# Performance work log

Hardware: AMD Instinct MI355X
Metric: run time of the kernel (lower is better)

Reference implementation:

```python
import jax, jax.numpy as jnp
import numpy as np
import math

S, B, H, NH = 2048, 1, 4096, 32
HD = H // NH          # 128 head dim
ROT = HD // 2         # 64 rotary dim per half (position_encoding_2d)


def _rotary_tables(seq_len):
    inv_freq = 1.0 / (10000.0 ** (jnp.arange(0, ROT, 2, dtype=jnp.float32) / ROT))  # [ROT/2]
    t = jnp.arange(seq_len, dtype=jnp.float32)
    freqs = jnp.einsum('i,j->ij', t, inv_freq)          # [S, ROT/2]
    emb = jnp.concatenate([freqs, freqs], axis=-1)       # [S, ROT]
    return jnp.cos(emb), jnp.sin(emb)


def _rotate_half(x):
    half = x.shape[-1] // 2
    return jnp.concatenate([-x[..., half:], x[..., :half]], axis=-1)


def _apply_rotary(q, k, cos, sin, pos):
    # q,k: [s,b,nh,ROT]; pos: [s,b]
    c = cos[pos][:, :, None, :]   # [s,b,1,ROT]
    s_ = sin[pos][:, :, None, :]
    return q * c + _rotate_half(q) * s_, k * c + _rotate_half(k) * s_


def reference(hidden_states, position_ids, attention_mask, layer_id, w_qkv, b_qkv, w_dense, b_dense):
    s, b, _ = hidden_states.shape
    # fused QKV projection (Linear: x @ W.T + b)
    qkv = jnp.einsum('sbh,oh->sbo', hidden_states, w_qkv) + b_qkv     # [s,b,3H]
    qkv = qkv.reshape(s, b, NH, 3 * HD)
    q, k, v = jnp.split(qkv, 3, axis=-1)                               # each [s,b,nh,HD]
    # 2D rotary: split head dim in two halves, rotate with pos / block pos ids
    cos, sin = _rotary_tables(s)
    pos = position_ids[:, 0, :].T        # [s,b]
    blk = position_ids[:, 1, :].T        # [s,b]
    q1, q2 = jnp.split(q, 2, axis=-1)
    k1, k2 = jnp.split(k, 2, axis=-1)
    q1, k1 = _apply_rotary(q1, k1, cos, sin, pos)
    q2, k2 = _apply_rotary(q2, k2, cos, sin, blk)
    q = jnp.concatenate([q1, q2], axis=-1)
    k = jnp.concatenate([k1, k2], axis=-1)
    # layer-id-dependent scaling (GLM numerics): q scaled down by coeff, logits scaled back up
    coeff = float(layer_id + 1)
    q = q / (math.sqrt(HD) * coeff)
    scores = jnp.einsum('sbnd,tbnd->bnst', q, k)                       # [b,nh,s,s]
    scores = jnp.where(attention_mask, jnp.asarray(-10000.0, scores.dtype), scores)
    probs = jax.nn.softmax(scores.astype(jnp.float32) * coeff, axis=-1).astype(scores.dtype)
    ctx = jnp.einsum('bnst,tbnd->sbnd', probs, v).reshape(s, b, H)     # [s,b,H]
    return jnp.einsum('sbh,oh->sbo', ctx, w_dense) + b_dense


def setup_inputs() -> dict:
    key = jax.random.key(0)
    k1, k2, k3, k4, k5, k6 = jax.random.split(key, 6)
    init = 0.02
    hidden_states = jax.random.normal(k1, (S, B, H), dtype=jnp.float32)
    # GLM-style 2D position ids: [B, 2, S] (row 0: positions, row 1: block positions)
    pos = jnp.broadcast_to(jnp.arange(S, dtype=jnp.int64), (B, S))
    blk = jnp.broadcast_to(jnp.arange(S, dtype=jnp.int64), (B, S))
    position_ids = jnp.stack([pos, blk], axis=1)                        # [B,2,S]
    # causal mask: True = masked (future positions)
    causal = jnp.triu(jnp.ones((S, S), dtype=bool), k=1)
    attention_mask = jnp.broadcast_to(causal[None, None], (B, 1, S, S))
    return {
        'hidden_states': hidden_states,
        'position_ids': position_ids,
        'attention_mask': attention_mask,
        'layer_id': 5,
        'w_qkv': jax.random.normal(k2, (3 * H, H), dtype=jnp.float32) * init,
        'b_qkv': jax.random.normal(k3, (3 * H,), dtype=jnp.float32) * init,
        'w_dense': jax.random.normal(k4, (H, H), dtype=jnp.float32) * init,
        'b_dense': jax.random.normal(k5, (H,), dtype=jnp.float32) * init,
    }
```

## Files before the change

kernel.cpp:

```cpp
#include <hip/hip_runtime.h>
#include <math.h>
#include <stdint.h>

constexpr int S  = 2048;
constexpr int H  = 4096;
constexpr int NH = 32;
constexpr int HD = 128;
constexpr int H3 = 3 * H;

typedef unsigned short u16;
typedef __bf16 bf16x8 __attribute__((ext_vector_type(8)));
typedef float  f32x4  __attribute__((ext_vector_type(4)));
typedef unsigned short us8 __attribute__((ext_vector_type(8)));

__device__ __forceinline__ u16 f2bf(float f) {
  uint32_t u = __float_as_uint(f);
  uint32_t r = (u + 0x7fff + ((u >> 16) & 1)) >> 16;
  return (u16)r;
}
__device__ __forceinline__ float bf2f(u16 u) {
  return __uint_as_float((uint32_t)u << 16);
}

__device__ __forceinline__ void load_lds16(const void* g, void* l) {
  __builtin_amdgcn_global_load_lds(
      (__attribute__((address_space(1))) void*)(uintptr_t)g,
      (__attribute__((address_space(3))) void*)l,
      16, 0, 0);
}

#define SBAR0 __builtin_amdgcn_sched_barrier(0)

__global__ __launch_bounds__(256)
void cast_all(const float* __restrict__ w_qkv, const float* __restrict__ hidden,
              const float* __restrict__ w_dense, u16* __restrict__ wq,
              u16* __restrict__ hb, u16* __restrict__ wd) {
  constexpr int NQ  = H3 * H / 4;
  constexpr int NHd = S * H / 4;
  constexpr int ND  = H * H / 4;
  constexpr int NT  = NQ + NHd + ND;
  for (int i = blockIdx.x * 256 + threadIdx.x; i < NT; i += gridDim.x * 256) {
    const float4* src;
    ushort4* dst;
    int j = i;
    if (j < NQ)            { src = (const float4*)w_qkv;  dst = (ushort4*)wq; }
    else if (j < NQ + NHd) { j -= NQ; src = (const float4*)hidden; dst = (ushort4*)hb; }
    else                   { j -= NQ + NHd; src = (const float4*)w_dense; dst = (ushort4*)wd; }
    float4 v = src[j];
    ushort4 o;
    o.x = f2bf(v.x); o.y = f2bf(v.y); o.z = f2bf(v.z); o.w = f2bf(v.w);
    dst[j] = o;
  }
}

template<int STRIDE, int OUT_BF16>
__global__ __launch_bounds__(512, 2)
void gemm256(const u16* __restrict__ A, const u16* __restrict__ W,
             const float* __restrict__ bias, void* __restrict__ Cout) {
  constexpr int K   = 4096;
  constexpr int NT  = K / 64;
  constexpr int NTM = 8;
  constexpr int TB  = 65536;
  __shared__ __attribute__((aligned(16))) unsigned char lds[2 * TB];
  const int tid = threadIdx.x, wave = tid >> 6, lane = tid & 63;
  const int l15 = lane & 15, l4 = lane >> 4;
  const int wr = wave >> 2, wc = wave & 3;

  const int nwg = gridDim.x, bid = blockIdx.x;
  const int cpx = nwg >> 3;
  const int swz = (bid & 7) * cpx + (bid >> 3);
  const int bx = swz / NTM, by = swz - bx * NTM;
  const int bm = by * 256, bn = bx * 256;

  const int srow = lane >> 3;
  const int sck  = ((lane & 7) ^ srow) * 8;
  const u16* Abase = A + (size_t)(bm + srow) * K + sck;
  const u16* Wbase = W + (size_t)(bn + srow) * K + sck;

  auto stageU = [&](int tt, int u) {
    const int b = tt & 1;
    if (u < 4) {
      const int rb = u * 64 + wave * 8;
      load_lds16(Abase + (size_t)rb * K + tt * 64, &lds[b * TB + rb * 128]);
    } else {
      const int rb = (u - 4) * 64 + wave * 8;
      load_lds16(Wbase + (size_t)rb * K + tt * 64,
                 &lds[b * TB + 32768 + rb * 128]);
    }
  };

  f32x4 acc[8][4];
#pragma unroll
  for (int i = 0; i < 8; ++i)
#pragma unroll
    for (int j = 0; j < 4; ++j) acc[i][j] = (f32x4)0.f;

#pragma unroll
  for (int u = 0; u < 8; ++u) stageU(0, u);
#pragma unroll
  for (int u = 0; u < 8; ++u) stageU(1, u);
  asm volatile("s_waitcnt vmcnt(8)" ::: "memory");
  SBAR0;
  __builtin_amdgcn_s_barrier();

  const int arow = wr * 128 + l15;
  const int brow = wc * 64 + l15;
  const int ckx  = l15 & 7;

  bf16x8 af[4][2], bfA[2][2], bfB[2][2];

  for (int t = 0; t < NT; ++t) {
    const int b0 = (t & 1) * TB;
    const bool st = (t + 2 < NT);
#pragma unroll
    for (int mi = 0; mi < 4; ++mi)
#pragma unroll
      for (int ks = 0; ks < 2; ++ks)
        af[mi][ks] = *(const bf16x8*)&lds[b0 + (arow + mi * 16) * 128 +
                                          (((ks * 4 + l4) ^ ckx) * 16)];
#pragma unroll
    for (int ni = 0; ni < 2; ++ni)
#pragma unroll
      for (int ks = 0; ks < 2; ++ks)
        bfA[ni][ks] = *(const bf16x8*)&lds[b0 + 32768 + (brow + ni * 16) * 128 +
                                           (((ks * 4 + l4) ^ ckx) * 16)];
    SBAR0; __builtin_amdgcn_s_barrier();
    asm volatile("s_waitcnt lgkmcnt(0)" ::: "memory");
    SBAR0;
    __builtin_amdgcn_s_setprio(1);
#pragma unroll
    for (int ks = 0; ks < 2; ++ks)
#pragma unroll
      for (int mi = 0; mi < 4; ++mi)
#pragma unroll
        for (int ni = 0; ni < 2; ++ni)
          acc[mi][ni] = __builtin_amdgcn_mfma_f32_16x16x32_bf16(af[mi][ks], bfA[ni][ks], acc[mi][ni], 0, 0, 0);
    __builtin_amdgcn_s_setprio(0);
    SBAR0; __builtin_amdgcn_s_barrier();
#pragma unroll
    for (int ni = 0; ni < 2; ++ni)
#pragma unroll
      for (int ks = 0; ks < 2; ++ks)
        bfB[ni][ks] = *(const bf16x8*)&lds[b0 + 32768 + (brow + (ni + 2) * 16) * 128 +
                                           (((ks * 4 + l4) ^ ckx) * 16)];
    if (st) { stageU(t + 2, 0); stageU(t + 2, 2); }
    SBAR0; __builtin_amdgcn_s_barrier();
    asm volatile("s_waitcnt lgkmcnt(0)" ::: "memory");
    SBAR0;
    __builtin_amdgcn_s_setprio(1);
#pragma unroll
    for (int ks = 0; ks < 2; ++ks)
#pragma unroll
      for (int mi = 0; mi < 4; ++mi)
#pragma unroll
        for (int ni = 0; ni < 2; ++ni)
          acc[mi][ni + 2] = __builtin_amdgcn_mfma_f32_16x16x32_bf16(af[mi][ks], bfB[ni][ks], acc[mi][ni + 2], 0, 0, 0);
    __builtin_amdgcn_s_setprio(0);
    SBAR0; __builtin_amdgcn_s_barrier();
#pragma unroll
    for (int mi = 0; mi < 4; ++mi)
#pragma unroll
      for (int ks = 0; ks < 2; ++ks)
        af[mi][ks] = *(const bf16x8*)&lds[b0 + (arow + (mi + 4) * 16) * 128 +
                                          (((ks * 4 + l4) ^ ckx) * 16)];
    if (st) { stageU(t + 2, 4); stageU(t + 2, 5); }
    SBAR0; __builtin_amdgcn_s_barrier();
    asm volatile("s_waitcnt lgkmcnt(0)" ::: "memory");
    SBAR0;
    __builtin_amdgcn_s_setprio(1);
#pragma unroll
    for (int ks = 0; ks < 2; ++ks)
#pragma unroll
      for (int mi = 0; mi < 4; ++mi)
#pragma unroll
        for (int ni = 0; ni < 2; ++ni)
          acc[mi + 4][ni] = __builtin_amdgcn_mfma_f32_16x16x32_bf16(af[mi][ks], bfA[ni][ks], acc[mi + 4][ni], 0, 0, 0);
    __builtin_amdgcn_s_setprio(0);
    SBAR0; __builtin_amdgcn_s_barrier();
    if (st) { stageU(t + 2, 1); stageU(t + 2, 3); stageU(t + 2, 6); stageU(t + 2, 7); }
    SBAR0;
    __builtin_amdgcn_s_setprio(1);
#pragma unroll
    for (int ks = 0; ks < 2; ++ks)
#pragma unroll
      for (int mi = 0; mi < 4; ++mi)
#pragma unroll
        for (int ni = 0; ni < 2; ++ni)
          acc[mi + 4][ni + 2] = __builtin_amdgcn_mfma_f32_16x16x32_bf16(af[mi][ks], bfB[ni][ks], acc[mi + 4][ni + 2], 0, 0, 0);
    __builtin_amdgcn_s_setprio(0);
    if (t < NT - 2)       asm volatile("s_waitcnt vmcnt(8)" ::: "memory");
    else if (t == NT - 2) asm volatile("s_waitcnt vmcnt(0)" ::: "memory");
    SBAR0;
    if (t < NT - 1) __builtin_amdgcn_s_barrier();
  }

#pragma unroll
  for (int ni = 0; ni < 4; ++ni) {
    const int col = bn + wc * 64 + ni * 16 + l15;
    const float bv = bias[col];
#pragma unroll
    for (int mi = 0; mi < 8; ++mi) {
#pragma unroll
      for (int r = 0; r < 4; ++r) {
        const int row = bm + wr * 128 + mi * 16 + l4 * 4 + r;
        const float v = acc[mi][ni][r] + bv;
        if (OUT_BF16) ((u16*)Cout)[(size_t)row * STRIDE + col] = f2bf(v);
        else          ((float*)Cout)[(size_t)row * STRIDE + col] = v;
      }
    }
  }
}

template<int STRIDE, int OUT_BF16>
__global__ __launch_bounds__(512, 2)
void gemm8p(const u16* __restrict__ A, const u16* __restrict__ W,
            const float* __restrict__ bias, void* __restrict__ Cout) {
  constexpr int K  = 4096;
  constexpr int NT = K / 64;
  constexpr int NTM = 16;
  constexpr int TB = 49152;
  __shared__ __attribute__((aligned(16))) unsigned char lds[3 * TB];
  const int tid = threadIdx.x, wave = tid >> 6, lane = tid & 63;
  const int l15 = lane & 15, l4 = lane >> 4;
  const int wr = wave >> 2, wc = wave & 3;

  const int nwg = gridDim.x, bid = blockIdx.x;
  const int cpx = nwg >> 3;
  const int swz = (bid & 7) * cpx + (bid >> 3);
  const int bx = swz / NTM, by = swz - bx * NTM;
  const int bm = by * 128, bn = bx * 256;

  const int srow = lane >> 3;
  const int sck  = ((lane & 7) ^ srow) * 8;
  const u16* Abase = A + (size_t)(bm + srow) * K + sck;
  const u16* Wbase = W + (size_t)(bn + srow) * K + sck;

  auto stageA = [&](int tt, int b) {
#pragma unroll
    for (int j = 0; j < 2; ++j) {
      const int rb = j * 64 + wave * 8;
      load_lds16(Abase + (size_t)rb * K + tt * 64, &lds[b * TB + rb * 128]);
    }
  };
  auto stageB = [&](int tt, int b, int u) {
#pragma unroll
    for (int j = 0; j < 2; ++j) {
      const int rb = u * 128 + j * 64 + wave * 8;
      load_lds16(Wbase + (size_t)rb * K + tt * 64,
                 &lds[b * TB + 16384 + rb * 128]);
    }
  };

  f32x4 acc[4][4];
#pragma unroll
  for (int i = 0; i < 4; ++i)
#pragma unroll
    for (int j = 0; j < 4; ++j) acc[i][j] = (f32x4)0.f;

  stageA(0, 0); stageB(0, 0, 0); stageB(0, 0, 1);
  stageA(1, 1); stageB(1, 1, 0); stageB(1, 1, 1);
  asm volatile("s_waitcnt vmcnt(6)" ::: "memory");
  SBAR0;
  __builtin_amdgcn_s_barrier();

  const int arow = wr * 64 + l15;
  const int brow = wc * 64 + l15;
  const int ckx  = l15 & 7;

  bf16x8 af[4][2], bf[4][2];

  int br = 0, bs = 2;
  for (int t = 0; t < NT; ++t) {
    const int b0 = br * TB;
#pragma unroll
    for (int mi = 0; mi < 2; ++mi)
#pragma unroll
      for (int ks = 0; ks < 2; ++ks)
        af[mi][ks] = *(const bf16x8*)&lds[b0 + (arow + mi * 16) * 128 +
                                          (((ks * 4 + l4) ^ ckx) * 16)];
#pragma unroll
    for (int ni = 0; ni < 2; ++ni)
#pragma unroll
      for (int ks = 0; ks < 2; ++ks)
        bf[ni][ks] = *(const bf16x8*)&lds[b0 + 16384 + (brow + ni * 16) * 128 +
                                          (((ks * 4 + l4) ^ ckx) * 16)];
    if (t < NT - 2) stageA(t + 2, bs);
    SBAR0; __builtin_amdgcn_s_barrier();
    asm volatile("s_waitcnt lgkmcnt(0)" ::: "memory");
    SBAR0;
    __builtin_amdgcn_s_setprio(1);
#pragma unroll
    for (int ks = 0; ks < 2; ++ks)
#pragma unroll
      for (int mi = 0; mi < 2; ++mi)
#pragma unroll
        for (int ni = 0; ni < 2; ++ni)
          acc[mi][ni] = __builtin_amdgcn_mfma_f32_16x16x32_bf16(af[mi][ks], bf[ni][ks], acc[mi][ni], 0, 0, 0);
    __builtin_amdgcn_s_setprio(0);
    SBAR0; __builtin_amdgcn_s_barrier();
#pragma unroll
    for (int ni = 2; ni < 4; ++ni)
#pragma unroll
      for (int ks = 0; ks < 2; ++ks)
        bf[ni][ks] = *(const bf16x8*)&lds[b0 + 16384 + (brow + ni * 16) * 128 +
                                          (((ks * 4 + l4) ^ ckx) * 16)];
    if (t < NT - 2) stageB(t + 2, bs, 0);
    SBAR0; __builtin_amdgcn_s_barrier();
    asm volatile("s_waitcnt lgkmcnt(0)" ::: "memory");
    SBAR0;
    __builtin_amdgcn_s_setprio(1);
#pragma unroll
    for (int ks = 0; ks < 2; ++ks)
#pragma unroll
      for (int mi = 0; mi < 2; ++mi)
#pragma unroll
        for (int ni = 2; ni < 4; ++ni)
          acc[mi][ni] = __builtin_amdgcn_mfma_f32_16x16x32_bf16(af[mi][ks], bf[ni][ks], acc[mi][ni], 0, 0, 0);
    __builtin_amdgcn_s_setprio(0);
    SBAR0; __builtin_amdgcn_s_barrier();
#pragma unroll
    for (int mi = 2; mi < 4; ++mi)
#pragma unroll
      for (int ks = 0; ks < 2; ++ks)
        af[mi][ks] = *(const bf16x8*)&lds[b0 + (arow + mi * 16) * 128 +
                                          (((ks * 4 + l4) ^ ckx) * 16)];
    if (t < NT - 2) stageB(t + 2, bs, 1);
    SBAR0; __builtin_amdgcn_s_barrier();
    asm volatile("s_waitcnt lgkmcnt(0)" ::: "memory");
    SBAR0;
    __builtin_amdgcn_s_setprio(1);
#pragma unroll
    for (int ks = 0; ks < 2; ++ks)
#pragma unroll
      for (int mi = 2; mi < 4; ++mi)
#pragma unroll
        for (int ni = 0; ni < 2; ++ni)
          acc[mi][ni] = __builtin_amdgcn_mfma_f32_16x16x32_bf16(af[mi][ks], bf[ni][ks], acc[mi][ni], 0, 0, 0);
    __builtin_amdgcn_s_setprio(0);
    SBAR0; __builtin_amdgcn_s_barrier();
    __builtin_amdgcn_s_setprio(1);
#pragma unroll
    for (int ks = 0; ks < 2; ++ks)
#pragma unroll
      for (int mi = 2; mi < 4; ++mi)
#pragma unroll
        for (int ni = 2; ni < 4; ++ni)
          acc[mi][ni] = __builtin_amdgcn_mfma_f32_16x16x32_bf16(af[mi][ks], bf[ni][ks], acc[mi][ni], 0, 0, 0);
    __builtin_amdgcn_s_setprio(0);
    if (t < NT - 1) {
      if (t < NT - 2) asm volatile("s_waitcnt vmcnt(6)" ::: "memory");
      else            asm volatile("s_waitcnt vmcnt(0)" ::: "memory");
      SBAR0;
      __builtin_amdgcn_s_barrier();
    }
    br = (br == 2) ? 0 : br + 1;
    bs = (bs == 2) ? 0 : bs + 1;
  }

#pragma unroll
  for (int ni = 0; ni < 4; ++ni) {
    const int col = bn + wc * 64 + ni * 16 + l15;
    const float bv = bias[col];
#pragma unroll
    for (int mi = 0; mi < 4; ++mi) {
#pragma unroll
      for (int r = 0; r < 4; ++r) {
        const int row = bm + wr * 64 + mi * 16 + l4 * 4 + r;
        const float v = acc[mi][ni][r] + bv;
        if (OUT_BF16) ((u16*)Cout)[(size_t)row * STRIDE + col] = f2bf(v);
        else          ((float*)Cout)[(size_t)row * STRIDE + col] = v;
      }
    }
  }
}

__global__ __launch_bounds__(256)
void rotary_fused(const u16* __restrict__ qkv,
                  u16* __restrict__ Qb, u16* __restrict__ Kb,
                  u16* __restrict__ Vt) {
  __shared__ u16 vt[64][136];
  __shared__ float2 cs_tab[64][32];
  const int s0 = blockIdx.x * 64, h = blockIdx.y;
  const int tid = threadIdx.x;

  for (int idx = tid; idx < 2048; idx += 256) {
    const int r = idx >> 5, j = idx & 31;
    const float invf = exp2f(-(float)j * (13.287712379549449f / 32.f));
    float sn, c;
    sincosf((float)(s0 + r) * invf, &sn, &c);
    cs_tab[r][j] = make_float2(c, sn);
  }
  for (int idx = tid; idx < 1024; idx += 256) {
    const int r = idx >> 4, ck = idx & 15;
    us8 v = *(const us8*)(qkv + (size_t)(s0 + r) * H3 + h * 384 + 256 + ck * 8);
    *(us8*)&vt[r][ck * 8] = v;
  }
  __syncthreads();

  for (int idx = tid; idx < 2048; idx += 256) {
    const int r  = idx >> 5;
    const int sub = idx & 31;
    const int tq = sub >> 4;
    const int ck = sub & 15;
    const int s = s0 + r;
    const u16* base = qkv + (size_t)s * H3 + h * 384 + tq * 128;
    us8 v = *(const us8*)(base + ck * 8);
    us8 p = *(const us8*)(base + ((ck * 8) ^ 32));
    const int d0 = ck * 8;
    const float sign = ((d0 & 63) < 32) ? -1.f : 1.f;
    const float sc = tq ? 1.f : 0.12751721769218683f;
    us8 o;
#pragma unroll
    for (int e = 0; e < 8; ++e) {
      const float2 cs = cs_tab[r][(d0 + e) & 31];
      o[e] = f2bf((bf2f(v[e]) * cs.x + sign * bf2f(p[e]) * cs.y) * sc);
    }
    *(us8*)((tq ? Kb : Qb) + ((size_t)h * S + s) * HD + d0) = o;
  }
  for (int idx = tid; idx < 1024; idx += 256) {
    const int d = idx >> 3, c8 = idx & 7;
    us8 o;
#pragma unroll
    for (int e = 0; e < 8; ++e) o[e] = vt[c8 * 8 + e][d];
    *(us8*)(Vt + ((size_t)h * HD + d) * S + s0 + c8 * 8) = o;
  }
}

__global__ __launch_bounds__(256)
void attn(const u16* __restrict__ Qb, const u16* __restrict__ Kb,
          const u16* __restrict__ Vt, u16* __restrict__ ctx) {
  __shared__ __attribute__((aligned(16))) unsigned char sK[64 * 256];
  __shared__ __attribute__((aligned(16))) unsigned char sV[128 * 128];
  __shared__ __attribute__((aligned(16))) unsigned char sP[4][16 * 128];
  const int bid = blockIdx.x;
  const int ixd = bid >> 3;
  const int h   = (bid & 7) * 4 + (ixd & 3);
  const int p   = ixd >> 2;
  const int g   = p >> 3, a = p & 7;
  const int qb  = 8 * g + ((g & 1) ? 7 - a : a);
  const int tid = threadIdx.x, wave = tid >> 6, lane = tid & 63;
  const int l15 = lane & 15, l4 = lane >> 4;
  const int qw0 = qb * 64 + wave * 16;

  auto stage = [&](int it) {
    const int t0 = it * 64;
#pragma unroll
    for (int c = 0; c < 4; ++c) {
      const int rbase = c * 16 + wave * 4;
      const int rr = rbase + (lane >> 4);
      const int pp = lane & 15;
      load_lds16(Kb + ((size_t)h * S + t0 + rr) * HD + ((pp ^ (rr & 15)) * 8),
                 &sK[rbase * 256]);
    }
#pragma unroll
    for (int c = 0; c < 4; ++c) {
      const int rbase = c * 32 + wave * 8;
      const int rr = rbase + (lane >> 3);
      const int pp = lane & 7;
      load_lds16(Vt + ((size_t)h * HD + rr) * S + t0 + ((pp ^ (rr & 7)) * 8),
                 &sV[rbase * 128]);
    }
  };

  bf16x8 qf[4];
  {
    const u16* qrow = Qb + ((size_t)h * S + qw0 + l15) * HD;
#pragma unroll
    for (int ks = 0; ks < 4; ++ks)
      qf[ks] = *(const bf16x8*)(qrow + ks * 32 + l4 * 8);
  }

  f32x4 of[8];
#pragma unroll
  for (int i = 0; i < 8; ++i) of[i] = (f32x4)0.f;
  float mrun[4] = {-1e30f, -1e30f, -1e30f, -1e30f};
  float lrun[4] = {0.f, 0.f, 0.f, 0.f};

  const int nt = qb + 1;
  stage(0);
  for (int it = 0; it < nt; ++it) {
    const int t0 = it * 64;
    asm volatile("s_waitcnt vmcnt(0)" ::: "memory");
    SBAR0;
    __builtin_amdgcn_s_barrier();
    SBAR0;

    f32x4 sc[4];
#pragma unroll
    for (int nf = 0; nf < 4; ++nf) sc[nf] = (f32x4)0.f;
#pragma unroll
    for (int nf = 0; nf < 4; ++nf) {
      const int trow = nf * 16 + l15;
#pragma unroll
      for (int ks = 0; ks < 4; ++ks) {
        const int chunk = ks * 4 + l4;
        bf16x8 kf = *(const bf16x8*)&sK[trow * 256 + ((chunk ^ (trow & 15)) * 16)];
        sc[nf] = __builtin_amdgcn_mfma_f32_16x16x32_bf16(qf[ks], kf, sc[nf], 0, 0, 0);
      }
    }

    if (it == qb) {
#pragma unroll
      for (int nf = 0; nf < 4; ++nf) {
        const int tg = t0 + nf * 16 + l15;
#pragma unroll
        for (int r = 0; r < 4; ++r) {
          const int sg = qw0 + l4 * 4 + r;
          if (tg > sg) sc[nf][r] = -1e30f;
        }
      }
    }

    f32x4 vm = sc[0];
#pragma unroll
    for (int nf = 1; nf < 4; ++nf)
#pragma unroll
      for (int r = 0; r < 4; ++r) vm[r] = fmaxf(vm[r], sc[nf][r]);
#pragma unroll
    for (int m = 1; m <= 8; m <<= 1)
#pragma unroll
      for (int r = 0; r < 4; ++r) vm[r] = fmaxf(vm[r], __shfl_xor(vm[r], m, 64));

    bool need = false;
#pragma unroll
    for (int r = 0; r < 4; ++r) need = need || (vm[r] > mrun[r] + 8.f);
    if (__builtin_amdgcn_ballot_w64(need)) {
#pragma unroll
      for (int r = 0; r < 4; ++r) {
        const float nm = fmaxf(mrun[r], vm[r]);
        const float scale = exp2f(mrun[r] - nm);
        mrun[r] = nm;
        lrun[r] *= scale;
#pragma unroll
        for (int i = 0; i < 8; ++i) of[i][r] *= scale;
      }
    }

    f32x4 rs = (f32x4)0.f;
#pragma unroll
    for (int nf = 0; nf < 4; ++nf) {
#pragma unroll
      for (int r = 0; r < 4; ++r) {
        const float pv = exp2f(sc[nf][r] - mrun[r]);
        rs[r] += pv;
        const int row = l4 * 4 + r;
        const int t = nf * 16 + l15;
        const int chunk = t >> 3;
        *(u16*)&sP[wave][row * 128 + ((chunk ^ (row & 7)) * 16) + (t & 7) * 2] = f2bf(pv);
      }
    }
#pragma unroll
    for (int m = 1; m <= 8; m <<= 1)
#pragma unroll
      for (int r = 0; r < 4; ++r) rs[r] += __shfl_xor(rs[r], m, 64);
#pragma unroll
    for (int r = 0; r < 4; ++r) lrun[r] += rs[r];

    asm volatile("s_waitcnt lgkmcnt(0)" ::: "memory");
    SBAR0;

    bf16x8 pa[2];
#pragma unroll
    for (int ksP = 0; ksP < 2; ++ksP) {
      const int chunk = ksP * 4 + l4;
      pa[ksP] = *(const bf16x8*)&sP[wave][l15 * 128 + ((chunk ^ (l15 & 7)) * 16)];
    }
#pragma unroll
    for (int nf2 = 0; nf2 < 8; ++nf2) {
      const int d = nf2 * 16 + l15;
#pragma unroll
      for (int ksP = 0; ksP < 2; ++ksP) {
        const int chunk = ksP * 4 + l4;
        bf16x8 vf = *(const bf16x8*)&sV[d * 128 + ((chunk ^ (d & 7)) * 16)];
        of[nf2] = __builtin_amdgcn_mfma_f32_16x16x32_bf16(pa[ksP], vf, of[nf2], 0, 0, 0);
      }
    }
    SBAR0;
    __builtin_amdgcn_s_barrier();
    if (it + 1 < nt) stage(it + 1);
  }

  float invr[4];
#pragma unroll
  for (int r = 0; r < 4; ++r) invr[r] = 1.f / lrun[r];
#pragma unroll
  for (int nf2 = 0; nf2 < 8; ++nf2) {
    const int d = nf2 * 16 + l15;
#pragma unroll
    for (int r = 0; r < 4; ++r) {
      const int srow = qw0 + l4 * 4 + r;
      ctx[(size_t)srow * H + h * HD + d] = f2bf(of[nf2][r] * invr[r]);
    }
  }
}

extern "C" void kernel_launch(void* const* d_in, const int* in_sizes, int n_in,
                              void* d_out, int out_size, void* d_ws, size_t ws_size,
                              hipStream_t stream) {
  (void)in_sizes; (void)n_in; (void)out_size; (void)ws_size;
  const float* hidden  = (const float*)d_in[0];
  const float* w_qkv   = (const float*)d_in[4];
  const float* b_qkv   = (const float*)d_in[5];
  const float* w_dense = (const float*)d_in[6];
  const float* b_dense = (const float*)d_in[7];
  float* out = (float*)d_out;

  char* ws = (char*)d_ws;
  u16* wqkvb   = (u16*)(ws + 0);
  u16* ctxb    = (u16*)(ws + 41943040);
  u16* hb      = (u16*)(ws + 100663296);
  u16* qkvb    = (u16*)(ws + 117440512);
  u16* Qbp     = (u16*)(ws + 167772160);
  u16* Kbp     = (u16*)(ws + 184549376);
  u16* Vtp     = (u16*)(ws + 201326592);
  u16* wdenseb = (u16*)(ws + 218103808);

  cast_all<<<2048, 256, 0, stream>>>(w_qkv, hidden, w_dense, wqkvb, hb, wdenseb);
  gemm256<H3, 1><<<dim3(256), 512, 0, stream>>>(hb, wqkvb, b_qkv, qkvb);
  gemm8p<H3, 1><<<dim3(256), 512, 0, stream>>>(
      hb, wqkvb + (size_t)8192 * 4096, b_qkv + 8192, (u16*)qkvb + 8192);
  rotary_fused<<<dim3(S / 64, NH), 256, 0, stream>>>(qkvb, Qbp, Kbp, Vtp);
  attn<<<dim3(1024), 256, 0, stream>>>(Qbp, Kbp, Vtp, ctxb);
  gemm8p<H, 0><<<dim3(256), 512, 0, stream>>>(ctxb, wdenseb, b_dense, out);
}
```

Baseline: 444.4 us.

## Reshape 8-phase GEMM tile to 256x128 with two-phase A-split pipeline

Replaces the 128x256 gemm8p kernel with a 256x128 tile variant, so each wave computes a 128x32 sub-tile (8x2 MFMA fragments) instead of 64x64. The four-phase load/compute schedule becomes two phases: all B fragments plus half of A, then the other half of A. Global-to-LDS staging is redistributed to match. This changes operand reuse and the ratio of LDS reads to MFMAs, and is used for both the tail of the QKV projection and the dense projection. Fewer barriers per iteration, but more A fragment loads per wave.

```diff
diff --git a/kernel.cpp b/kernel.cpp
--- a/kernel.cpp
+++ b/kernel.cpp
@@ -213,12 +213,12 @@
 
 template<int STRIDE, int OUT_BF16>
 __global__ __launch_bounds__(512, 2)
-void gemm8p(const u16* __restrict__ A, const u16* __restrict__ W,
-            const float* __restrict__ bias, void* __restrict__ Cout) {
-  constexpr int K  = 4096;
-  constexpr int NT = K / 64;
-  constexpr int NTM = 16;
-  constexpr int TB = 49152;
+void gemm256n(const u16* __restrict__ A, const u16* __restrict__ W,
+              const float* __restrict__ bias, void* __restrict__ Cout) {
+  constexpr int K   = 4096;
+  constexpr int NT  = K / 64;
+  constexpr int NTM = 8;
+  constexpr int TB  = 49152;
   __shared__ __attribute__((aligned(16))) unsigned char lds[3 * TB];
   const int tid = threadIdx.x, wave = tid >> 6, lane = tid & 63;
   const int l15 = lane & 15, l4 = lane >> 4;
@@ -228,52 +228,50 @@
   const int cpx = nwg >> 3;
   const int swz = (bid & 7) * cpx + (bid >> 3);
   const int bx = swz / NTM, by = swz - bx * NTM;
-  const int bm = by * 128, bn = bx * 256;
+  const int bm = by * 256, bn = bx * 128;
 
   const int srow = lane >> 3;
   const int sck  = ((lane & 7) ^ srow) * 8;
   const u16* Abase = A + (size_t)(bm + srow) * K + sck;
   const u16* Wbase = W + (size_t)(bn + srow) * K + sck;
 
-  auto stageA = [&](int tt, int b) {
-#pragma unroll
-    for (int j = 0; j < 2; ++j) {
-      const int rb = j * 64 + wave * 8;
+  auto stageU = [&](int tt, int b, int u) {
+    if (u < 4) {
+      const int rb = u * 64 + wave * 8;
       load_lds16(Abase + (size_t)rb * K + tt * 64, &lds[b * TB + rb * 128]);
+    } else {
+      const int rb = (u - 4) * 64 + wave * 8;
+      load_lds16(Wbase + (size_t)rb * K + tt * 64,
+                 &lds[b * TB + 32768 + rb * 128]);
     }
   };
-  auto stageB = [&](int tt, int b, int u) {
-#pragma unroll
-    for (int j = 0; j < 2; ++j) {
-      const int rb = u * 128 + j * 64 + wave * 8;
-      load_lds16(Wbase + (size_t)rb * K + tt * 64,
-                 &lds[b * TB + 16384 + rb * 128]);
-    }
-  };
-
-  f32x4 acc[4][4];
-#pragma unroll
-  for (int i = 0; i < 4; ++i)
-#pragma unroll
-    for (int j = 0; j < 4; ++j) acc[i][j] = (f32x4)0.f;
-
-  stageA(0, 0); stageB(0, 0, 0); stageB(0, 0, 1);
-  stageA(1, 1); stageB(1, 1, 0); stageB(1, 1, 1);
+
+  f32x4 acc[8][2];
+#pragma unroll
+  for (int i = 0; i < 8; ++i)
+#pragma unroll
+    for (int j = 0; j < 2; ++j) acc[i][j] = (f32x4)0.f;
+
+#pragma unroll
+  for (int u = 0; u < 6; ++u) stageU(0, 0, u);
+#pragma unroll
+  for (int u = 0; u < 6; ++u) stageU(1, 1, u);
   asm volatile("s_waitcnt vmcnt(6)" ::: "memory");
   SBAR0;
   __builtin_amdgcn_s_barrier();
 
-  const int arow = wr * 64 + l15;
-  const int brow = wc * 64 + l15;
+  const int arow = wr * 128 + l15;
+  const int brow = wc * 32 + l15;
   const int ckx  = l15 & 7;
 
-  bf16x8 af[4][2], bf[4][2];
+  bf16x8 af[4][2], bf[2][2];
 
   int br = 0, bs = 2;
   for (int t = 0; t < NT; ++t) {
     const int b0 = br * TB;
-#pragma unroll
-    for (int mi = 0; mi < 2; ++mi)
+    const bool st = (t + 2 < NT);
+#pragma unroll
+    for (int mi = 0; mi < 4; ++mi)
 #pragma unroll
       for (int ks = 0; ks < 2; ++ks)
         af[mi][ks] = *(const bf16x8*)&lds[b0 + (arow + mi * 16) * 128 +
@@ -282,9 +280,9 @@
     for (int ni = 0; ni < 2; ++ni)
 #pragma unroll
       for (int ks = 0; ks < 2; ++ks)
-        bf[ni][ks] = *(const bf16x8*)&lds[b0 + 16384 + (brow + ni * 16) * 128 +
+        bf[ni][ks] = *(const bf16x8*)&lds[b0 + 32768 + (brow + ni * 16) * 128 +
                                           (((ks * 4 + l4) ^ ckx) * 16)];
-    if (t < NT - 2) stageA(t + 2, bs);
+    if (st) { stageU(t + 2, bs, 0); stageU(t + 2, bs, 1); stageU(t + 2, bs, 4); }
     SBAR0; __builtin_amdgcn_s_barrier();
     asm volatile("s_waitcnt lgkmcnt(0)" ::: "memory");
     SBAR0;
@@ -292,19 +290,19 @@
 #pragma unroll
     for (int ks = 0; ks < 2; ++ks)
 #pragma unroll
-      for (int mi = 0; mi < 2; ++mi)
+      for (int mi = 0; mi < 4; ++mi)
 #pragma unroll
         for (int ni = 0; ni < 2; ++ni)
           acc[mi][ni] = __builtin_amdgcn_mfma_f32_16x16x32_bf16(af[mi][ks], bf[ni][ks], acc[mi][ni], 0, 0, 0);
     __builtin_amdgcn_s_setprio(0);
     SBAR0; __builtin_amdgcn_s_barrier();
 #pragma unroll
-    for (int ni = 2; ni < 4; ++ni)
-#pragma unroll
-      for (int ks = 0; ks < 2; ++ks)
-        bf[ni][ks] = *(const bf16x8*)&lds[b0 + 16384 + (brow + ni * 16) * 128 +
+    for (int mi = 0; mi < 4; ++mi)
+#pragma unroll
+      for (int ks = 0; ks < 2; ++ks)
+        af[mi][ks] = *(const bf16x8*)&lds[b0 + (arow + (mi + 4) * 16) * 128 +
                                           (((ks * 4 + l4) ^ ckx) * 16)];
-    if (t < NT - 2) stageB(t + 2, bs, 0);
+    if (st) { stageU(t + 2, bs, 2); stageU(t + 2, bs, 3); stageU(t + 2, bs, 5); }
     SBAR0; __builtin_amdgcn_s_barrier();
     asm volatile("s_waitcnt lgkmcnt(0)" ::: "memory");
     SBAR0;
@@ -312,40 +310,10 @@
 #pragma unroll
     for (int ks = 0; ks < 2; ++ks)
 #pragma unroll
-      for (int mi = 0; mi < 2; ++mi)
-#pragma unroll
-        for (int ni = 2; ni < 4; ++ni)
-          acc[mi][ni] = __builtin_amdgcn_mfma_f32_16x16x32_bf16(af[mi][ks], bf[ni][ks], acc[mi][ni], 0, 0, 0);
-    __builtin_amdgcn_s_setprio(0);
-    SBAR0; __builtin_amdgcn_s_barrier();
-#pragma unroll
-    for (int mi = 2; mi < 4; ++mi)
-#pragma unroll
-      for (int ks = 0; ks < 2; ++ks)
-        af[mi][ks] = *(const bf16x8*)&lds[b0 + (arow + mi * 16) * 128 +
-                                          (((ks * 4 + l4) ^ ckx) * 16)];
-    if (t < NT - 2) stageB(t + 2, bs, 1);
-    SBAR0; __builtin_amdgcn_s_barrier();
-    asm volatile("s_waitcnt lgkmcnt(0)" ::: "memory");
-    SBAR0;
-    __builtin_amdgcn_s_setprio(1);
-#pragma unroll
-    for (int ks = 0; ks < 2; ++ks)
-#pragma unroll
-      for (int mi = 2; mi < 4; ++mi)
+      for (int mi = 0; mi < 4; ++mi)
 #pragma unroll
         for (int ni = 0; ni < 2; ++ni)
-          acc[mi][ni] = __builtin_amdgcn_mfma_f32_16x16x32_bf16(af[mi][ks], bf[ni][ks], acc[mi][ni], 0, 0, 0);
-    __builtin_amdgcn_s_setprio(0);
-    SBAR0; __builtin_amdgcn_s_barrier();
-    __builtin_amdgcn_s_setprio(1);
-#pragma unroll
-    for (int ks = 0; ks < 2; ++ks)
-#pragma unroll
-      for (int mi = 2; mi < 4; ++mi)
-#pragma unroll
-        for (int ni = 2; ni < 4; ++ni)
-          acc[mi][ni] = __builtin_amdgcn_mfma_f32_16x16x32_bf16(af[mi][ks], bf[ni][ks], acc[mi][ni], 0, 0, 0);
+          acc[mi + 4][ni] = __builtin_amdgcn_mfma_f32_16x16x32_bf16(af[mi][ks], bf[ni][ks], acc[mi + 4][ni], 0, 0, 0);
     __builtin_amdgcn_s_setprio(0);
     if (t < NT - 1) {
       if (t < NT - 2) asm volatile("s_waitcnt vmcnt(6)" ::: "memory");
@@ -358,14 +326,14 @@
   }
 
 #pragma unroll
-  for (int ni = 0; ni < 4; ++ni) {
-    const int col = bn + wc * 64 + ni * 16 + l15;
+  for (int ni = 0; ni < 2; ++ni) {
+    const int col = bn + wc * 32 + ni * 16 + l15;
     const float bv = bias[col];
 #pragma unroll
-    for (int mi = 0; mi < 4; ++mi) {
+    for (int mi = 0; mi < 8; ++mi) {
 #pragma unroll
       for (int r = 0; r < 4; ++r) {
-        const int row = bm + wr * 64 + mi * 16 + l4 * 4 + r;
+        const int row = bm + wr * 128 + mi * 16 + l4 * 4 + r;
         const float v = acc[mi][ni][r] + bv;
         if (OUT_BF16) ((u16*)Cout)[(size_t)row * STRIDE + col] = f2bf(v);
         else          ((float*)Cout)[(size_t)row * STRIDE + col] = v;
@@ -617,9 +585,9 @@
 
   cast_all<<<2048, 256, 0, stream>>>(w_qkv, hidden, w_dense, wqkvb, hb, wdenseb);
   gemm256<H3, 1><<<dim3(256), 512, 0, stream>>>(hb, wqkvb, b_qkv, qkvb);
-  gemm8p<H3, 1><<<dim3(256), 512, 0, stream>>>(
+  gemm256n<H3, 1><<<dim3(256), 512, 0, stream>>>(
       hb, wqkvb + (size_t)8192 * 4096, b_qkv + 8192, (u16*)qkvb + 8192);
   rotary_fused<<<dim3(S / 64, NH), 256, 0, stream>>>(qkvb, Qbp, Kbp, Vtp);
   attn<<<dim3(1024), 256, 0, stream>>>(Qbp, Kbp, Vtp, ctxb);
-  gemm8p<H, 0><<<dim3(256), 512, 0, stream>>>(ctxb, wdenseb, b_dense, out);
-}
+  gemm256n<H, 0><<<dim3(256), 512, 0, stream>>>(ctxb, wdenseb, b_dense, out);
+}
```

Measured after the change: 452.1 us. Within noise of the previous version (+1.7%).
